# Kernel optimization log

Hardware: AMD Instinct MI355X
Metric: run time of the kernel (lower is better)

Reference implementation:

```python
import jax, jax.numpy as jnp
import numpy as np

AUDIO_DIM, TEXT_DIM, HIDDEN_DIM = 512, 768, 512
B, AUDIO_LEN, TEXT_LEN = 8, 2048, 512


def setup_inputs() -> dict:
    key = jax.random.key(0)
    ks = jax.random.split(key, 9)
    audio_features = jax.random.normal(ks[0], (B, AUDIO_LEN, AUDIO_DIM), dtype=jnp.float32)
    text_features = jax.random.normal(ks[1], (B, TEXT_LEN, TEXT_DIM), dtype=jnp.float32)
    text_mask = jax.random.randint(ks[2], (B, TEXT_LEN), 0, 2).astype(jnp.int32)
    # Linear params (PyTorch default init scale ~ U(-1/sqrt(fan_in), 1/sqrt(fan_in)))
    def lin(kw, kb, fan_in, fan_out):
        bound = 1.0 / np.sqrt(fan_in)
        W = jax.random.uniform(kw, (fan_in, fan_out), minval=-bound, maxval=bound, dtype=jnp.float32)
        b = jax.random.uniform(kb, (fan_out,), minval=-bound, maxval=bound, dtype=jnp.float32)
        return W, b
    Wq, bq = lin(ks[3], ks[4], AUDIO_DIM, HIDDEN_DIM)
    Wk, bk = lin(ks[5], ks[6], TEXT_DIM, HIDDEN_DIM)
    Wv, bv = lin(ks[7], ks[8], TEXT_DIM, HIDDEN_DIM)
    return {
        "audio_features": audio_features,
        "text_features": text_features,
        "Wq": Wq, "bq": bq, "Wk": Wk, "bk": bk, "Wv": Wv, "bv": bv,
        "text_mask": text_mask,
    }


def reference(audio_features, text_features, Wq, bq, Wk, bk, Wv, bv, text_mask):
    scale = HIDDEN_DIM ** -0.5
    q = jnp.einsum("bad,dh->bah", audio_features, Wq) + bq  # (B, A, H)
    k = jnp.einsum("btd,dh->bth", text_features, Wk) + bk   # (B, T, H)
    v = jnp.einsum("btd,dh->bth", text_features, Wv) + bv   # (B, T, H)
    scores = jnp.einsum("bah,bth->bat", q, k) * scale        # (B, A, T)
    mask = text_mask[:, None, :]  # (B, 1, T)
    scores = jnp.where(mask == 0, -jnp.inf, scores)
    attn = jax.nn.softmax(scores, axis=-1)
    # dropout is identity in eval mode
    enhanced_audio = jnp.einsum("bat,bth->bah", attn, v)     # (B, A, H)
    return enhanced_audio
```

## Files before the change

### kernel.cpp

```cpp
#include <hip/hip_runtime.h>
#include <cstdint>
#include <cstddef>

#define AUDIO_DIM 512
#define TEXT_DIM  768
#define HIDDEN    512
#define BATCH     8
#define ALEN      2048
#define TLEN      512

typedef _Float16 half8 __attribute__((ext_vector_type(8)));
typedef _Float16 half4_t __attribute__((ext_vector_type(4)));
typedef float floatx4 __attribute__((ext_vector_type(4)));

#define AS1 __attribute__((address_space(1)))
#define AS3 __attribute__((address_space(3)))

__device__ __forceinline__ void gload_lds16(const void* g, void* l) {
    __builtin_amdgcn_global_load_lds((const AS1 void*)g, (AS3 void*)l, 16, 0, 0);
}

__device__ __forceinline__ int swz(int r) { return (r >> 1) & 3; }

__global__ __launch_bounds__(256) void prep(
    const float* __restrict__ audio, const float* __restrict__ text,
    const float* __restrict__ Wq, const float* __restrict__ Wk,
    const float* __restrict__ Wv,
    _Float16* __restrict__ audio_h, _Float16* __restrict__ text_h,
    _Float16* __restrict__ Wq_t, _Float16* __restrict__ Wk_t,
    _Float16* __restrict__ Wv_t)
{
    __shared__ _Float16 tt[32 * 33];
    const int bid = blockIdx.x, tid = threadIdx.x;
    if (bid < 11264) {
        const float* src; _Float16* dst; int i;
        if (bid < 8192) { src = audio; dst = audio_h; i = bid * 256 + tid; }
        else            { src = text;  dst = text_h;  i = (bid - 8192) * 256 + tid; }
        float4 v = ((const float4*)src)[i];
        half4_t h;
        h.x = (_Float16)v.x; h.y = (_Float16)v.y; h.z = (_Float16)v.z; h.w = (_Float16)v.w;
        ((half4_t*)dst)[i] = h;
    } else {
        const float* src; _Float16* dst; int R, lb;
        if (bid < 11520)      { lb = bid - 11264; src = Wq; dst = Wq_t; R = 512; }
        else if (bid < 11904) { lb = bid - 11520; src = Wk; dst = Wk_t; R = 768; }
        else                  { lb = bid - 11904; src = Wv; dst = Wv_t; R = 768; }
        const int C = 512;
        const int c0 = (lb & 15) * 32, r0 = (lb >> 4) * 32;
        const int tx = tid & 31, ty = tid >> 5;
#pragma unroll
        for (int i = 0; i < 4; i++) {
            int r = ty + i * 8;
            tt[r * 33 + tx] = (_Float16)src[(size_t)(r0 + r) * C + c0 + tx];
        }
        __syncthreads();
#pragma unroll
        for (int i = 0; i < 4; i++) {
            int r = ty + i * 8;
            dst[(size_t)(c0 + r) * R + r0 + tx] = tt[tx * 33 + r];
        }
    }
}

template <bool OUT16, bool ROWBIAS>
__device__ __forceinline__ void gemm_body(
    const _Float16* __restrict__ A, const _Float16* __restrict__ Bt,
    const float* __restrict__ bias, void* __restrict__ Cp,
    int N, int K, int m0, int n0, _Float16* Asm, _Float16* Bsm)
{
    const int tid = threadIdx.x;
    const int l = tid & 63, w = tid >> 6;
    const int wm = w >> 1, wn = w & 1;
    const int srow = l >> 2, sj = l & 3;
    const int q = l >> 4, c16 = l & 15;

    floatx4 acc[4][4] = {};

    for (int k0 = 0; k0 < K; k0 += 32) {
        if (k0) __syncthreads();
#pragma unroll
        for (int i = 0; i < 2; i++) {
            int rb = (w * 2 + i) * 16;
            int r = rb + srow;
            int cc = sj ^ swz(r);
            gload_lds16(A + (size_t)(m0 + r) * K + k0 + cc * 8, Asm + rb * 32);
            gload_lds16(Bt + (size_t)(n0 + r) * K + k0 + cc * 8, Bsm + rb * 32);
        }
        __syncthreads();

        half8 af[4], bf[4];
#pragma unroll
        for (int t = 0; t < 4; t++) {
            int rA = wm * 64 + t * 16 + c16;
            af[t] = *(const half8*)&Asm[rA * 32 + ((q ^ swz(rA)) << 3)];
            int rB = wn * 64 + t * 16 + c16;
            bf[t] = *(const half8*)&Bsm[rB * 32 + ((q ^ swz(rB)) << 3)];
        }
#pragma unroll
        for (int mi = 0; mi < 4; mi++)
#pragma unroll
            for (int ni = 0; ni < 4; ni++)
                acc[mi][ni] = __builtin_amdgcn_mfma_f32_16x16x32_f16(
                    af[mi], bf[ni], acc[mi][ni], 0, 0, 0);
    }

    if (OUT16) {
        float bcol[4];
        float brow[4][4];
        if (!ROWBIAS) {
#pragma unroll
            for (int ni = 0; ni < 4; ni++)
                bcol[ni] = bias[n0 + wn * 64 + ni * 16 + c16];
        } else {
#pragma unroll
            for (int mi = 0; mi < 4; mi++) {
                float4 b4 = *(const float4*)&bias[m0 + wm * 64 + mi * 16 + q * 4];
                brow[mi][0] = b4.x; brow[mi][1] = b4.y;
                brow[mi][2] = b4.z; brow[mi][3] = b4.w;
            }
        }
        _Float16* C = (_Float16*)Cp;
#pragma unroll
        for (int ni = 0; ni < 4; ni++) {
            int col = n0 + wn * 64 + ni * 16 + c16;
#pragma unroll
            for (int mi = 0; mi < 4; mi++) {
                int row = m0 + wm * 64 + mi * 16 + q * 4;
#pragma unroll
                for (int r = 0; r < 4; r++) {
                    float b = ROWBIAS ? brow[mi][r] : bcol[ni];
                    C[(size_t)(row + r) * N + col] = (_Float16)(acc[mi][ni][r] + b);
                }
            }
        }
    } else {
        float* C = (float*)Cp;
#pragma unroll
        for (int ni = 0; ni < 4; ni++) {
            int col = n0 + wn * 64 + ni * 16 + c16;
#pragma unroll
            for (int mi = 0; mi < 4; mi++) {
                int row = m0 + wm * 64 + mi * 16 + q * 4;
#pragma unroll
                for (int r = 0; r < 4; r++)
                    C[(size_t)(row + r) * N + col] = acc[mi][ni][r];
            }
        }
    }
}

__global__ __launch_bounds__(256, 2) void qkv_gemm(
    const _Float16* __restrict__ audio_h, const _Float16* __restrict__ text_h,
    const _Float16* __restrict__ Wq_t, const _Float16* __restrict__ Wk_t,
    const _Float16* __restrict__ Wv_t,
    const float* __restrict__ bq, const float* __restrict__ bk,
    const float* __restrict__ bv,
    _Float16* __restrict__ Qh, _Float16* __restrict__ Kh,
    _Float16* __restrict__ Vt)
{
    __shared__ __align__(16) _Float16 Asm[128 * 32];
    __shared__ __align__(16) _Float16 Bsm[128 * 32];
    const int bid = blockIdx.x;
    if (bid < 512) {
        gemm_body<true, false>(audio_h, Wq_t, bq, Qh, 512, 512,
                               (bid >> 2) * 128, (bid & 3) * 128, Asm, Bsm);
    } else if (bid < 640) {
        int lb = bid - 512;
        gemm_body<true, false>(text_h, Wk_t, bk, Kh, 512, 768,
                               (lb >> 2) * 128, (lb & 3) * 128, Asm, Bsm);
    } else {
        int lb = bid - 640;
        int z = lb >> 4, by = (lb >> 2) & 3, bx = lb & 3;
        gemm_body<true, true>(Wv_t, text_h + (size_t)z * 393216, bv,
                              Vt + (size_t)z * 262144, 512, 768,
                              by * 128, bx * 128, Asm, Bsm);
    }
}

__global__ __launch_bounds__(256, 2) void pv_gemm(
    const _Float16* __restrict__ P, const _Float16* __restrict__ Vt,
    float* __restrict__ out)
{
    __shared__ __align__(16) _Float16 Asm[128 * 32];
    __shared__ __align__(16) _Float16 Bsm[128 * 32];
    const int z = blockIdx.z;
    gemm_body<false, false>(P + (size_t)z * 1048576, Vt + (size_t)z * 262144,
                            nullptr, out + (size_t)z * 1048576, 512, 512,
                            blockIdx.y * 128, blockIdx.x * 128, Asm, Bsm);
}

__global__ __launch_bounds__(256, 2) void scores_softmax(
    const _Float16* __restrict__ Qh, const _Float16* __restrict__ Kh,
    const int* __restrict__ mask, _Float16* __restrict__ P) {
    __shared__ __align__(16) _Float16 Qs[64 * 32];
    __shared__ __align__(16) _Float16 Ks[512 * 32];
    __shared__ float red[4][64];
    __shared__ float red2[4][64];
    const int tid = threadIdx.x, l = tid & 63, w = tid >> 6;
    const int b = blockIdx.y, a0 = blockIdx.x * 64;
    const _Float16* Qb = Qh + (size_t)(b * ALEN + a0) * HIDDEN;
    const _Float16* Kb = Kh + (size_t)b * TLEN * HIDDEN;
    const int srow = l >> 2, sj = l & 3;
    const int q = l >> 4, c16 = l & 15;

    floatx4 acc[4][8] = {};

    for (int k0 = 0; k0 < HIDDEN; k0 += 32) {
        if (k0) __syncthreads();
        {
            int rb = w * 16;
            int r = rb + srow;
            int cc = sj ^ swz(r);
            gload_lds16(Qb + (size_t)r * HIDDEN + k0 + cc * 8, &Qs[rb * 32]);
        }
#pragma unroll
        for (int i = 0; i < 8; i++) {
            int rb = (w * 8 + i) * 16;
            int r = rb + srow;
            int cc = sj ^ swz(r);
            gload_lds16(Kb + (size_t)r * HIDDEN + k0 + cc * 8, &Ks[rb * 32]);
        }
        __syncthreads();

        half8 af[4], bf[8];
#pragma unroll
        for (int t = 0; t < 4; t++) {
            int rA = t * 16 + c16;
            af[t] = *(const half8*)&Qs[rA * 32 + ((q ^ swz(rA)) << 3)];
        }
#pragma unroll
        for (int t = 0; t < 8; t++) {
            int rB = w * 128 + t * 16 + c16;
            bf[t] = *(const half8*)&Ks[rB * 32 + ((q ^ swz(rB)) << 3)];
        }
#pragma unroll
        for (int mi = 0; mi < 4; mi++)
#pragma unroll
            for (int ni = 0; ni < 8; ni++)
                acc[mi][ni] = __builtin_amdgcn_mfma_f32_16x16x32_f16(
                    af[mi], bf[ni], acc[mi][ni], 0, 0, 0);
    }

    const float scale = 0.044194173824159216f;
    int mv[8];
#pragma unroll
    for (int ni = 0; ni < 8; ni++)
        mv[ni] = mask[b * TLEN + w * 128 + ni * 16 + c16];
#pragma unroll
    for (int mi = 0; mi < 4; mi++)
#pragma unroll
        for (int ni = 0; ni < 8; ni++)
#pragma unroll
            for (int r = 0; r < 4; r++)
                acc[mi][ni][r] = mv[ni] ? acc[mi][ni][r] * scale : -1e30f;

    float mx[4][4];
#pragma unroll
    for (int mi = 0; mi < 4; mi++)
#pragma unroll
        for (int r = 0; r < 4; r++) {
            float m = -1e30f;
#pragma unroll
            for (int ni = 0; ni < 8; ni++) m = fmaxf(m, acc[mi][ni][r]);
#pragma unroll
            for (int off = 1; off <= 8; off <<= 1) m = fmaxf(m, __shfl_xor(m, off));
            mx[mi][r] = m;
        }
    if (c16 == 0)
#pragma unroll
        for (int mi = 0; mi < 4; mi++)
#pragma unroll
            for (int r = 0; r < 4; r++) red[w][mi * 16 + q * 4 + r] = mx[mi][r];
    __syncthreads();
#pragma unroll
    for (int mi = 0; mi < 4; mi++)
#pragma unroll
        for (int r = 0; r < 4; r++) {
            int row = mi * 16 + q * 4 + r;
            mx[mi][r] = fmaxf(fmaxf(red[0][row], red[1][row]),
                              fmaxf(red[2][row], red[3][row]));
        }

    float sm[4][4];
#pragma unroll
    for (int mi = 0; mi < 4; mi++)
#pragma unroll
        for (int r = 0; r < 4; r++) {
            float s = 0.f;
#pragma unroll
            for (int ni = 0; ni < 8; ni++) {
                float e = __expf(acc[mi][ni][r] - mx[mi][r]);
                acc[mi][ni][r] = e;
                s += e;
            }
#pragma unroll
            for (int off = 1; off <= 8; off <<= 1) s += __shfl_xor(s, off);
            sm[mi][r] = s;
        }
    if (c16 == 0)
#pragma unroll
        for (int mi = 0; mi < 4; mi++)
#pragma unroll
            for (int r = 0; r < 4; r++) red2[w][mi * 16 + q * 4 + r] = sm[mi][r];
    __syncthreads();

    _Float16* Pb = P + (size_t)(b * ALEN + a0) * TLEN;
#pragma unroll
    for (int mi = 0; mi < 4; mi++)
#pragma unroll
        for (int r = 0; r < 4; r++) {
            int row = mi * 16 + q * 4 + r;
            float inv = 1.f / (red2[0][row] + red2[1][row] + red2[2][row] + red2[3][row]);
#pragma unroll
            for (int ni = 0; ni < 8; ni++)
                Pb[(size_t)row * TLEN + w * 128 + ni * 16 + c16] =
                    (_Float16)(acc[mi][ni][r] * inv);
        }
}

extern "C" void kernel_launch(void* const* d_in, const int* in_sizes, int n_in,
                              void* d_out, int out_size, void* d_ws, size_t ws_size,
                              hipStream_t stream)
{
    const float* audio = (const float*)d_in[0];
    const float* text  = (const float*)d_in[1];
    const float* Wq    = (const float*)d_in[2];
    const float* bq    = (const float*)d_in[3];
    const float* Wk    = (const float*)d_in[4];
    const float* bk    = (const float*)d_in[5];
    const float* Wv    = (const float*)d_in[6];
    const float* bv    = (const float*)d_in[7];
    const int*   maskp = (const int*)d_in[8];
    float* out = (float*)d_out;

    _Float16* audio_h = (_Float16*)d_out;
    _Float16* Qh      = audio_h + (size_t)8388608;

    _Float16* ws16   = (_Float16*)d_ws;
    _Float16* text_h = ws16;
    _Float16* Wq_t   = text_h + 3145728;
    _Float16* Wk_t   = Wq_t + 262144;
    _Float16* Wv_t   = Wk_t + 393216;
    _Float16* Kh     = Wv_t + 393216;
    _Float16* Vt     = Kh + 2097152;
    _Float16* P      = Vt + 2097152;

    prep<<<12288, 256, 0, stream>>>(audio, text, Wq, Wk, Wv,
                                    audio_h, text_h, Wq_t, Wk_t, Wv_t);
    qkv_gemm<<<768, 256, 0, stream>>>(audio_h, text_h, Wq_t, Wk_t, Wv_t,
                                      bq, bk, bv, Qh, Kh, Vt);
    scores_softmax<<<dim3(32, 8), 256, 0, stream>>>(Qh, Kh, maskp, P);
    pv_gemm<<<dim3(4, 16, 8), 256, 0, stream>>>(P, Vt, out);
}
```

Before: 177.1 us.

## Fuse scores, softmax and PV GEMM into one attention kernel

Merges the scores/softmax kernel and the PV GEMM into a single kernel. The normalized probability tile is kept in swizzled LDS and multiplied against V tiles streamed from global memory, so the fp16 P matrix is never written to or read back from global memory, and one kernel launch is removed. The query tile shrinks from 64 to 32 rows, which doubles the grid and the number of times K and V are reloaded per batch. Qh moves into the workspace slot that P used to occupy.

```diff
diff --git a/kernel.cpp b/kernel.cpp
--- a/kernel.cpp
+++ b/kernel.cpp
@@ -177,64 +177,58 @@
     }
 }
 
-__global__ __launch_bounds__(256, 2) void pv_gemm(
-    const _Float16* __restrict__ P, const _Float16* __restrict__ Vt,
+#define QT 32
+#define PSTR 544
+
+__global__ __launch_bounds__(256, 2) void attn_fused(
+    const _Float16* __restrict__ Qh, const _Float16* __restrict__ Kh,
+    const _Float16* __restrict__ Vt, const int* __restrict__ mask,
     float* __restrict__ out)
 {
-    __shared__ __align__(16) _Float16 Asm[128 * 32];
-    __shared__ __align__(16) _Float16 Bsm[128 * 32];
-    const int z = blockIdx.z;
-    gemm_body<false, false>(P + (size_t)z * 1048576, Vt + (size_t)z * 262144,
-                            nullptr, out + (size_t)z * 1048576, 512, 512,
-                            blockIdx.y * 128, blockIdx.x * 128, Asm, Bsm);
-}
-
-__global__ __launch_bounds__(256, 2) void scores_softmax(
-    const _Float16* __restrict__ Qh, const _Float16* __restrict__ Kh,
-    const int* __restrict__ mask, _Float16* __restrict__ P) {
-    __shared__ __align__(16) _Float16 Qs[64 * 32];
-    __shared__ __align__(16) _Float16 Ks[512 * 32];
-    __shared__ float red[4][64];
-    __shared__ float red2[4][64];
+    __shared__ __align__(16) _Float16 Qs[QT * 32];
+    __shared__ __align__(16) _Float16 KV[512 * 32];
+    __shared__ __align__(16) _Float16 Pl[QT * PSTR];
+    __shared__ float red[4][QT];
+    __shared__ float red2[4][QT];
     const int tid = threadIdx.x, l = tid & 63, w = tid >> 6;
-    const int b = blockIdx.y, a0 = blockIdx.x * 64;
+    const int b = blockIdx.y, a0 = blockIdx.x * QT;
     const _Float16* Qb = Qh + (size_t)(b * ALEN + a0) * HIDDEN;
     const _Float16* Kb = Kh + (size_t)b * TLEN * HIDDEN;
+    const _Float16* Vb = Vt + (size_t)b * HIDDEN * TLEN;
     const int srow = l >> 2, sj = l & 3;
     const int q = l >> 4, c16 = l & 15;
 
-    floatx4 acc[4][8] = {};
-
+    floatx4 acc[2][8] = {};
     for (int k0 = 0; k0 < HIDDEN; k0 += 32) {
         if (k0) __syncthreads();
-        {
+        if (w < 2) {
             int rb = w * 16;
             int r = rb + srow;
             int cc = sj ^ swz(r);
-            gload_lds16(Qb + (size_t)r * HIDDEN + k0 + cc * 8, &Qs[rb * 32]);
+            gload_lds16(Qb + (size_t)r * HIDDEN + k0 + cc * 8, Qs + rb * 32);
         }
 #pragma unroll
         for (int i = 0; i < 8; i++) {
             int rb = (w * 8 + i) * 16;
             int r = rb + srow;
             int cc = sj ^ swz(r);
-            gload_lds16(Kb + (size_t)r * HIDDEN + k0 + cc * 8, &Ks[rb * 32]);
+            gload_lds16(Kb + (size_t)r * HIDDEN + k0 + cc * 8, KV + rb * 32);
         }
         __syncthreads();
 
-        half8 af[4], bf[8];
-#pragma unroll
-        for (int t = 0; t < 4; t++) {
+        half8 af[2], bf[8];
+#pragma unroll
+        for (int t = 0; t < 2; t++) {
             int rA = t * 16 + c16;
             af[t] = *(const half8*)&Qs[rA * 32 + ((q ^ swz(rA)) << 3)];
         }
 #pragma unroll
         for (int t = 0; t < 8; t++) {
             int rB = w * 128 + t * 16 + c16;
-            bf[t] = *(const half8*)&Ks[rB * 32 + ((q ^ swz(rB)) << 3)];
-        }
-#pragma unroll
-        for (int mi = 0; mi < 4; mi++)
+            bf[t] = *(const half8*)&KV[rB * 32 + ((q ^ swz(rB)) << 3)];
+        }
+#pragma unroll
+        for (int mi = 0; mi < 2; mi++)
 #pragma unroll
             for (int ni = 0; ni < 8; ni++)
                 acc[mi][ni] = __builtin_amdgcn_mfma_f32_16x16x32_f16(
@@ -247,16 +241,16 @@
     for (int ni = 0; ni < 8; ni++)
         mv[ni] = mask[b * TLEN + w * 128 + ni * 16 + c16];
 #pragma unroll
-    for (int mi = 0; mi < 4; mi++)
+    for (int mi = 0; mi < 2; mi++)
 #pragma unroll
         for (int ni = 0; ni < 8; ni++)
 #pragma unroll
             for (int r = 0; r < 4; r++)
                 acc[mi][ni][r] = mv[ni] ? acc[mi][ni][r] * scale : -1e30f;
 
-    float mx[4][4];
-#pragma unroll
-    for (int mi = 0; mi < 4; mi++)
+    float mx[2][4];
+#pragma unroll
+    for (int mi = 0; mi < 2; mi++)
 #pragma unroll
         for (int r = 0; r < 4; r++) {
             float m = -1e30f;
@@ -268,12 +262,12 @@
         }
     if (c16 == 0)
 #pragma unroll
-        for (int mi = 0; mi < 4; mi++)
+        for (int mi = 0; mi < 2; mi++)
 #pragma unroll
             for (int r = 0; r < 4; r++) red[w][mi * 16 + q * 4 + r] = mx[mi][r];
     __syncthreads();
 #pragma unroll
-    for (int mi = 0; mi < 4; mi++)
+    for (int mi = 0; mi < 2; mi++)
 #pragma unroll
         for (int r = 0; r < 4; r++) {
             int row = mi * 16 + q * 4 + r;
@@ -281,9 +275,9 @@
                               fmaxf(red[2][row], red[3][row]));
         }
 
-    float sm[4][4];
-#pragma unroll
-    for (int mi = 0; mi < 4; mi++)
+    float sm[2][4];
+#pragma unroll
+    for (int mi = 0; mi < 2; mi++)
 #pragma unroll
         for (int r = 0; r < 4; r++) {
             float s = 0.f;
@@ -299,23 +293,71 @@
         }
     if (c16 == 0)
 #pragma unroll
-        for (int mi = 0; mi < 4; mi++)
+        for (int mi = 0; mi < 2; mi++)
 #pragma unroll
             for (int r = 0; r < 4; r++) red2[w][mi * 16 + q * 4 + r] = sm[mi][r];
     __syncthreads();
 
-    _Float16* Pb = P + (size_t)(b * ALEN + a0) * TLEN;
-#pragma unroll
-    for (int mi = 0; mi < 4; mi++)
+#pragma unroll
+    for (int mi = 0; mi < 2; mi++)
 #pragma unroll
         for (int r = 0; r < 4; r++) {
             int row = mi * 16 + q * 4 + r;
             float inv = 1.f / (red2[0][row] + red2[1][row] + red2[2][row] + red2[3][row]);
 #pragma unroll
+            for (int ni = 0; ni < 8; ni++) {
+                int t = w * 128 + ni * 16 + c16;
+                int chunk = t >> 3;
+                int chunkS = (chunk & ~3) | ((chunk & 3) ^ ((row >> 1) & 3));
+                Pl[row * PSTR + chunkS * 8 + (t & 7)] = (_Float16)(acc[mi][ni][r] * inv);
+            }
+        }
+    __syncthreads();
+
+    floatx4 oacc[2][8] = {};
+    for (int k0 = 0; k0 < TLEN; k0 += 32) {
+        if (k0) __syncthreads();
+#pragma unroll
+        for (int i = 0; i < 8; i++) {
+            int rb = (w * 8 + i) * 16;
+            int r = rb + srow;
+            int cc = sj ^ swz(r);
+            gload_lds16(Vb + (size_t)r * TLEN + k0 + cc * 8, KV + rb * 32);
+        }
+        __syncthreads();
+
+        half8 pf[2], vf[8];
+#pragma unroll
+        for (int mi = 0; mi < 2; mi++) {
+            int row = mi * 16 + c16;
+            int chunkS = (k0 >> 3) + (q ^ ((c16 >> 1) & 3));
+            pf[mi] = *(const half8*)&Pl[row * PSTR + chunkS * 8];
+        }
+#pragma unroll
+        for (int t = 0; t < 8; t++) {
+            int rB = w * 128 + t * 16 + c16;
+            vf[t] = *(const half8*)&KV[rB * 32 + ((q ^ swz(rB)) << 3)];
+        }
+#pragma unroll
+        for (int mi = 0; mi < 2; mi++)
+#pragma unroll
             for (int ni = 0; ni < 8; ni++)
-                Pb[(size_t)row * TLEN + w * 128 + ni * 16 + c16] =
-                    (_Float16)(acc[mi][ni][r] * inv);
-        }
+                oacc[mi][ni] = __builtin_amdgcn_mfma_f32_16x16x32_f16(
+                    pf[mi], vf[ni], oacc[mi][ni], 0, 0, 0);
+    }
+
+#pragma unroll
+    for (int ni = 0; ni < 8; ni++) {
+        int col = w * 128 + ni * 16 + c16;
+#pragma unroll
+        for (int mi = 0; mi < 2; mi++) {
+            int row = mi * 16 + q * 4;
+#pragma unroll
+            for (int r = 0; r < 4; r++)
+                out[(size_t)(b * ALEN + a0 + row + r) * HIDDEN + col] =
+                    oacc[mi][ni][r];
+        }
+    }
 }
 
 extern "C" void kernel_launch(void* const* d_in, const int* in_sizes, int n_in,
@@ -334,7 +376,6 @@
     float* out = (float*)d_out;
 
     _Float16* audio_h = (_Float16*)d_out;
-    _Float16* Qh      = audio_h + (size_t)8388608;
 
     _Float16* ws16   = (_Float16*)d_ws;
     _Float16* text_h = ws16;
@@ -343,12 +384,11 @@
     _Float16* Wv_t   = Wk_t + 393216;
     _Float16* Kh     = Wv_t + 393216;
     _Float16* Vt     = Kh + 2097152;
-    _Float16* P      = Vt + 2097152;
+    _Float16* Qh     = Vt + 2097152;
 
     prep<<<12288, 256, 0, stream>>>(audio, text, Wq, Wk, Wv,
                                     audio_h, text_h, Wq_t, Wk_t, Wv_t);
     qkv_gemm<<<768, 256, 0, stream>>>(audio_h, text_h, Wq_t, Wk_t, Wv_t,
                                       bq, bk, bv, Qh, Kh, Vt);
-    scores_softmax<<<dim3(32, 8), 256, 0, stream>>>(Qh, Kh, maskp, P);
-    pv_gemm<<<dim3(4, 16, 8), 256, 0, stream>>>(P, Vt, out);
-}
+    attn_fused<<<dim3(ALEN / QT, BATCH), 256, 0, stream>>>(Qh, Kh, Vt, maskp, out);
+}
```

After: 177.8 us. About the same (+0.4%).
